# Kernel tuning notes

Measured on AMD Instinct MI355X. Metric: run time of the kernel, lower is better.

## Reference

```python
import jax, jax.numpy as jnp
import numpy as np

N = 20000      # nodes
E = 640000     # edges
D_IN = 128
D_OUT = 128
EPS_LN = 1e-6


def setup_inputs() -> dict:
    key = jax.random.key(0)
    ks = jax.random.split(key, 12)
    h = jax.random.normal(ks[0], (N, D_IN), dtype=jnp.float32)
    r = jax.random.normal(ks[1], (E, D_IN), dtype=jnp.float32)
    src = jax.random.randint(ks[2], (E,), 0, N, dtype=jnp.int32)
    dst = jax.random.randint(ks[3], (E,), 0, N, dtype=jnp.int32)
    # LayerNorm params (head, tail, rel)
    hn_a = jnp.ones((D_IN,), jnp.float32); hn_b = jnp.zeros((D_IN,), jnp.float32)
    tn_a = jnp.ones((D_IN,), jnp.float32); tn_b = jnp.zeros((D_IN,), jnp.float32)
    rn_a = jnp.ones((D_IN,), jnp.float32); rn_b = jnp.zeros((D_IN,), jnp.float32)
    sc = 1.0 / np.sqrt(D_IN)
    head_w = jax.random.normal(ks[4], (D_IN,), jnp.float32) * sc
    tail_w = jax.random.normal(ks[5], (D_IN,), jnp.float32) * sc
    rel_w = jax.random.normal(ks[6], (D_IN,), jnp.float32) * sc
    fc_w = jax.random.normal(ks[7], (D_IN, D_OUT), jnp.float32) * sc
    fc_b = jnp.zeros((D_OUT,), jnp.float32)
    return {"h": h, "r": r, "src": src, "dst": dst,
            "hn_a": hn_a, "hn_b": hn_b, "tn_a": tn_a, "tn_b": tn_b,
            "rn_a": rn_a, "rn_b": rn_b,
            "head_w": head_w, "tail_w": tail_w, "rel_w": rel_w,
            "fc_w": fc_w, "fc_b": fc_b}


def _layer_norm(x, a, b):
    # faithful to torch: std with Bessel correction (unbiased), eps added to std
    mean = x.mean(axis=-1, keepdims=True)
    var = jnp.sum((x - mean) ** 2, axis=-1, keepdims=True) / (x.shape[-1] - 1)
    std = jnp.sqrt(var)
    return a * (x - mean) / (std + EPS_LN) + b


def reference(h, r, src, dst, hn_a, hn_b, tn_a, tn_b, rn_a, rn_b,
              head_w, tail_w, rel_w, fc_w, fc_b):
    # per-node / per-edge scalar attention logits
    eh = jnp.tanh(_layer_norm(h, hn_a, hn_b) @ head_w)   # [N]
    et = jnp.tanh(_layer_norm(h, tn_a, tn_b) @ tail_w)   # [N]
    er = jnp.tanh(_layer_norm(r, rn_a, rn_b) @ rel_w)    # [E]
    # edge attention: act(eh[src] + et[dst] + er), activation = relu
    e = jax.nn.relu(eh[src] + et[dst] + er)              # [E]
    # edge_softmax: softmax over incoming edges of each destination node
    emax = jax.ops.segment_max(e, dst, num_segments=N)   # [N]
    ex = jnp.exp(e - emax[dst])
    esum = jax.ops.segment_sum(ex, dst, num_segments=N)  # [N]
    a = ex / esum[dst]                                   # [E]
    # u_mul_e + sum aggregation: feat[v] = sum_{(u->v)} a_e * h[u]
    msg = h[src] * a[:, None]                            # [E, D_IN]
    feat = jax.ops.segment_sum(msg, dst, num_segments=N) # [N, D_IN]
    out = feat @ fc_w + fc_b                             # [N, D_OUT]
    # F.normalize(p=2, dim=1)
    nrm = jnp.sqrt(jnp.sum(out * out, axis=1, keepdims=True))
    return out / jnp.maximum(nrm, 1e-12)
```

## Files before the change

kernel.cpp:

```cpp
#include <hip/hip_runtime.h>
#include <stdint.h>

#define D_DIM 128
#define EPS_LN 1e-6f

__device__ __forceinline__ float tanh_fast(float x) {
    return 1.0f - 2.0f / (__expf(2.0f * x) + 1.0f);
}

__device__ __forceinline__ float wave_sum(float v) {
    #pragma unroll
    for (int m = 1; m < 64; m <<= 1) v += __shfl_xor(v, m, 64);
    return v;
}

__device__ __forceinline__ float group16_sum(float v) {
    #pragma unroll
    for (int m = 1; m < 16; m <<= 1) v += __shfl_xor(v, m, 64);
    return v;
}

__device__ __forceinline__ float dot8_ln(const float4& a, const float4& b,
                                         float mean, float inv,
                                         const float4& wa0, const float4& wa1,
                                         const float4& wb0, const float4& wb1,
                                         const float4& ww0, const float4& ww1) {
    float p = 0.0f;
    p += ((a.x - mean) * inv * wa0.x + wb0.x) * ww0.x;
    p += ((a.y - mean) * inv * wa0.y + wb0.y) * ww0.y;
    p += ((a.z - mean) * inv * wa0.z + wb0.z) * ww0.z;
    p += ((a.w - mean) * inv * wa0.w + wb0.w) * ww0.w;
    p += ((b.x - mean) * inv * wa1.x + wb1.x) * ww1.x;
    p += ((b.y - mean) * inv * wa1.y + wb1.y) * ww1.y;
    p += ((b.z - mean) * inv * wa1.z + wb1.z) * ww1.z;
    p += ((b.w - mean) * inv * wa1.w + wb1.w) * ww1.w;
    return p;
}

__global__ __launch_bounds__(256) void k_node(
    const float* __restrict__ h,
    const float* __restrict__ hn_a, const float* __restrict__ hn_b,
    const float* __restrict__ tn_a, const float* __restrict__ tn_b,
    const float* __restrict__ head_w, const float* __restrict__ tail_w,
    float* __restrict__ eh, float* __restrict__ et, int n)
{
    int gid  = blockIdx.x * 256 + threadIdx.x;
    int node = gid >> 4;
    int sub  = threadIdx.x & 15;
    if (node >= n) return;

    const float4* hp = (const float4*)(h + (size_t)node * 128);
    float4 a = hp[sub * 2], b = hp[sub * 2 + 1];

    float s  = a.x + a.y + a.z + a.w + b.x + b.y + b.z + b.w;
    float s2 = a.x*a.x + a.y*a.y + a.z*a.z + a.w*a.w
             + b.x*b.x + b.y*b.y + b.z*b.z + b.w*b.w;
    s  = group16_sum(s);
    s2 = group16_sum(s2);
    float mean = s * (1.0f / 128.0f);
    float var  = fmaxf((s2 - s * mean) * (1.0f / 127.0f), 0.0f);
    float inv  = 1.0f / (sqrtf(var) + EPS_LN);

    int i0 = sub * 2, i1 = sub * 2 + 1;
    float4 ha0 = ((const float4*)hn_a)[i0],  ha1 = ((const float4*)hn_a)[i1];
    float4 hb0 = ((const float4*)hn_b)[i0],  hb1 = ((const float4*)hn_b)[i1];
    float4 hw0 = ((const float4*)head_w)[i0],hw1 = ((const float4*)head_w)[i1];
    float4 ta0 = ((const float4*)tn_a)[i0],  ta1 = ((const float4*)tn_a)[i1];
    float4 tb0 = ((const float4*)tn_b)[i0],  tb1 = ((const float4*)tn_b)[i1];
    float4 tw0 = ((const float4*)tail_w)[i0],tw1 = ((const float4*)tail_w)[i1];

    float ph = dot8_ln(a, b, mean, inv, ha0, ha1, hb0, hb1, hw0, hw1);
    float pt = dot8_ln(a, b, mean, inv, ta0, ta1, tb0, tb1, tw0, tw1);
    ph = group16_sum(ph);
    pt = group16_sum(pt);

    if (sub == 0) {
        eh[node] = tanh_fast(ph);
        et[node] = tanh_fast(pt);
    }
}

__global__ __launch_bounds__(256) void k_edge(
    const float* __restrict__ r,
    const float* __restrict__ rn_a, const float* __restrict__ rn_b,
    const float* __restrict__ rel_w,
    const int* __restrict__ src, const int* __restrict__ dst,
    const float* __restrict__ eh, const float* __restrict__ et,
    float* __restrict__ e_x, int* __restrict__ cnt, int nE)
{
    int gid  = blockIdx.x * 256 + threadIdx.x;
    int edge = gid >> 4;
    int sub  = threadIdx.x & 15;
    if (edge >= nE) return;

    int sN = 0, dN = 0;
    float vh = 0.0f, vt = 0.0f;
    if (sub == 0) {
        sN = src[edge];
        dN = dst[edge];
        vh = eh[sN];
        vt = et[dN];
    }

    const float4* rp = (const float4*)(r + (size_t)edge * 128);
    float4 a = rp[sub * 2], b = rp[sub * 2 + 1];

    float s  = a.x + a.y + a.z + a.w + b.x + b.y + b.z + b.w;
    float s2 = a.x*a.x + a.y*a.y + a.z*a.z + a.w*a.w
             + b.x*b.x + b.y*b.y + b.z*b.z + b.w*b.w;
    s  = group16_sum(s);
    s2 = group16_sum(s2);
    float mean = s * (1.0f / 128.0f);
    float var  = fmaxf((s2 - s * mean) * (1.0f / 127.0f), 0.0f);
    float inv  = 1.0f / (sqrtf(var) + EPS_LN);

    int i0 = sub * 2, i1 = sub * 2 + 1;
    float4 ra0 = ((const float4*)rn_a)[i0],  ra1 = ((const float4*)rn_a)[i1];
    float4 rb0 = ((const float4*)rn_b)[i0],  rb1 = ((const float4*)rn_b)[i1];
    float4 rw0 = ((const float4*)rel_w)[i0], rw1 = ((const float4*)rel_w)[i1];

    float pr = dot8_ln(a, b, mean, inv, ra0, ra1, rb0, rb1, rw0, rw1);
    pr = group16_sum(pr);

    if (sub == 0) {
        float v = tanh_fast(pr) + vh + vt;
        v = fmaxf(v, 0.0f);
        e_x[edge] = __expf(v);
        atomicAdd(cnt + dN, 1);
    }
}

__global__ __launch_bounds__(1024) void k_scan(
    const int* __restrict__ cnt, int* __restrict__ off, int* __restrict__ cursor, int n)
{
    __shared__ int wsum[16];
    __shared__ int carry_s;
    int tid = threadIdx.x, lane = tid & 63, wid = tid >> 6;
    if (tid == 0) carry_s = 0;
    __syncthreads();
    int nC = (n + 1023) >> 10;
    for (int c = 0; c < nC; c++) {
        int i = (c << 10) + tid;
        int v = (i < n) ? cnt[i] : 0;
        int x = v;
        #pragma unroll
        for (int s = 1; s < 64; s <<= 1) {
            int t = __shfl_up(x, s, 64);
            if (lane >= s) x += t;
        }
        if (lane == 63) wsum[wid] = x;
        __syncthreads();
        if (wid == 0 && lane < 16) {
            int y = wsum[lane];
            #pragma unroll
            for (int s = 1; s < 16; s <<= 1) {
                int t = __shfl_up(y, s, 64);
                if (lane >= s) y += t;
            }
            wsum[lane] = y;
        }
        __syncthreads();
        int waveoff = (wid == 0) ? 0 : wsum[wid - 1];
        int excl = carry_s + waveoff + x - v;
        if (i < n) { off[i] = excl; cursor[i] = excl; }
        int tot = wsum[15];
        __syncthreads();
        if (tid == 0) carry_s += tot;
    }
    if (threadIdx.x == 0) off[n] = carry_s;
}

__global__ __launch_bounds__(256) void k_scatter(
    const int* __restrict__ src, const int* __restrict__ dst,
    const float* __restrict__ e_x, int* __restrict__ cursor,
    int* __restrict__ ssrc, float* __restrict__ sex, int nE)
{
    int e = blockIdx.x * 256 + threadIdx.x;
    if (e >= nE) return;
    int d = dst[e];
    int slot = atomicAdd(cursor + d, 1);
    ssrc[slot] = src[e];
    sex[slot]  = e_x[e];
}

__global__ __launch_bounds__(256) void k_agg(
    const float* __restrict__ h,
    const int* __restrict__ off,
    const int* __restrict__ ssrc, const float* __restrict__ sex,
    const float* __restrict__ fc_w, const float* __restrict__ fc_b,
    float* __restrict__ out, int n)
{
    __shared__ float feat[4][128];
    int wid = threadIdx.x >> 6, lane = threadIdx.x & 63;
    int v = blockIdx.x * 4 + wid;
    if (v >= n) return;

    int beg = off[v], end = off[v + 1];
    const float2* h2 = (const float2*)h;

    float acc0 = 0.0f, acc1 = 0.0f;
    float acc2 = 0.0f, acc3 = 0.0f;
    float ws0 = 0.0f, ws1 = 0.0f;

    for (int i = beg; i < end; i += 8) {
        int m = end - i;
        int   s_[8];
        float w_[8];
        float2 p_[8];
        #pragma unroll
        for (int j = 0; j < 8; j++) {
            if (j < m) { s_[j] = ssrc[i + j]; w_[j] = sex[i + j]; }
        }
        #pragma unroll
        for (int j = 0; j < 8; j++) {
            if (j < m) p_[j] = h2[(size_t)s_[j] * 64 + lane];
        }
        #pragma unroll
        for (int j = 0; j < 8; j += 2) {
            if (j < m) {
                acc0 += w_[j] * p_[j].x;
                acc1 += w_[j] * p_[j].y;
                ws0  += w_[j];
            }
            if (j + 1 < m) {
                acc2 += w_[j + 1] * p_[j + 1].x;
                acc3 += w_[j + 1] * p_[j + 1].y;
                ws1  += w_[j + 1];
            }
        }
    }
    acc0 += acc2; acc1 += acc3;
    float ws = ws0 + ws1;

    float inv = (end > beg) ? (1.0f / ws) : 0.0f;
    feat[wid][lane * 2]     = acc0 * inv;
    feat[wid][lane * 2 + 1] = acc1 * inv;

    const float2* w2 = (const float2*)fc_w;
    float2 bb = ((const float2*)fc_b)[lane];
    float o0 = bb.x, o1 = bb.y;
    #pragma unroll 8
    for (int d = 0; d < 128; d++) {
        float f = feat[wid][d];
        float2 ww = w2[d * 64 + lane];
        o0 += f * ww.x;
        o1 += f * ww.y;
    }

    float nrm2 = wave_sum(o0 * o0 + o1 * o1);
    float invn = 1.0f / fmaxf(sqrtf(nrm2), 1e-12f);
    o0 *= invn; o1 *= invn;
    float2 q; q.x = o0; q.y = o1;
    ((float2*)out)[(size_t)v * 64 + lane] = q;
}

extern "C" void kernel_launch(void* const* d_in, const int* in_sizes, int n_in,
                              void* d_out, int out_size, void* d_ws, size_t ws_size,
                              hipStream_t stream)
{
    const float* h      = (const float*)d_in[0];
    const float* r      = (const float*)d_in[1];
    const int*   src    = (const int*)d_in[2];
    const int*   dst    = (const int*)d_in[3];
    const float* hn_a   = (const float*)d_in[4];
    const float* hn_b   = (const float*)d_in[5];
    const float* tn_a   = (const float*)d_in[6];
    const float* tn_b   = (const float*)d_in[7];
    const float* rn_a   = (const float*)d_in[8];
    const float* rn_b   = (const float*)d_in[9];
    const float* head_w = (const float*)d_in[10];
    const float* tail_w = (const float*)d_in[11];
    const float* rel_w  = (const float*)d_in[12];
    const float* fc_w   = (const float*)d_in[13];
    const float* fc_b   = (const float*)d_in[14];

    int N = in_sizes[0] / D_DIM;
    int E = in_sizes[2];

    const int NA = 20480;
    float* base   = (float*)d_ws;
    float* eh     = base;
    float* et     = base + NA;
    int*   cnt    = (int*)(base + 2 * NA);
    int*   off    = (int*)(base + 3 * NA);
    int*   cursor = (int*)(base + 4 * NA);
    float* e_x    = base + 5 * NA;
    int*   ssrc   = (int*)(base + 5 * NA) + E;
    float* sex    = base + 5 * NA + 2 * E;

    hipMemsetAsync(cnt, 0, (size_t)NA * sizeof(int), stream);

    k_node<<<(N * 16 + 255) / 256, 256, 0, stream>>>(
        h, hn_a, hn_b, tn_a, tn_b, head_w, tail_w, eh, et, N);
    k_edge<<<(E * 16 + 255) / 256, 256, 0, stream>>>(
        r, rn_a, rn_b, rel_w, src, dst, eh, et, e_x, cnt, E);
    k_scan<<<1, 1024, 0, stream>>>(cnt, off, cursor, N);
    k_scatter<<<(E + 255) / 256, 256, 0, stream>>>(src, dst, e_x, cursor, ssrc, sex, E);
    k_agg<<<(N + 3) / 4, 256, 0, stream>>>(h, off, ssrc, sex, fc_w, fc_b,
                                           (float*)d_out, N);
}
```

Before: 645.1 us.

## Fuse all GNN stages into one cooperative persistent kernel with grid syncs

Merges the node-logit, edge-logit, scan, scatter and aggregation kernels plus the memset into a single cooperative launch. Grid-wide syncs separate the stages, and every stage uses grid-stride loops over an occupancy-sized grid. The edge pass now records each edge's atomic rank within its destination, so the scatter needs no second atomic. The single-block scan becomes a multi-block two-level scan, and source index and weight are packed into one int2 for the gather. This removes launch gaps and the serial scan, at the cost of five grid barriers and occupancy limited to what allows co-residency.

```diff
diff --git a/kernel.cpp b/kernel.cpp
--- a/kernel.cpp
+++ b/kernel.cpp
@@ -1,8 +1,12 @@
 #include <hip/hip_runtime.h>
+#include <hip/hip_cooperative_groups.h>
 #include <stdint.h>
+
+namespace cg = cooperative_groups;
 
 #define D_DIM 128
 #define EPS_LN 1e-6f
+#define NA 20480
 
 __device__ __forceinline__ float tanh_fast(float x) {
     return 1.0f - 2.0f / (__expf(2.0f * x) + 1.0f);
@@ -37,221 +41,220 @@
     return p;
 }
 
-__global__ __launch_bounds__(256) void k_node(
-    const float* __restrict__ h,
+__global__ __launch_bounds__(256) void k_fused(
+    const float* __restrict__ h, const float* __restrict__ r,
+    const int* __restrict__ src, const int* __restrict__ dst,
     const float* __restrict__ hn_a, const float* __restrict__ hn_b,
     const float* __restrict__ tn_a, const float* __restrict__ tn_b,
+    const float* __restrict__ rn_a, const float* __restrict__ rn_b,
     const float* __restrict__ head_w, const float* __restrict__ tail_w,
-    float* __restrict__ eh, float* __restrict__ et, int n)
+    const float* __restrict__ rel_w,
+    const float* __restrict__ fc_w, const float* __restrict__ fc_b,
+    float* __restrict__ out, float* __restrict__ ws,
+    int n, int nE)
 {
-    int gid  = blockIdx.x * 256 + threadIdx.x;
-    int node = gid >> 4;
-    int sub  = threadIdx.x & 15;
-    if (node >= n) return;
-
-    const float4* hp = (const float4*)(h + (size_t)node * 128);
-    float4 a = hp[sub * 2], b = hp[sub * 2 + 1];
-
-    float s  = a.x + a.y + a.z + a.w + b.x + b.y + b.z + b.w;
-    float s2 = a.x*a.x + a.y*a.y + a.z*a.z + a.w*a.w
-             + b.x*b.x + b.y*b.y + b.z*b.z + b.w*b.w;
-    s  = group16_sum(s);
-    s2 = group16_sum(s2);
-    float mean = s * (1.0f / 128.0f);
-    float var  = fmaxf((s2 - s * mean) * (1.0f / 127.0f), 0.0f);
-    float inv  = 1.0f / (sqrtf(var) + EPS_LN);
-
-    int i0 = sub * 2, i1 = sub * 2 + 1;
-    float4 ha0 = ((const float4*)hn_a)[i0],  ha1 = ((const float4*)hn_a)[i1];
-    float4 hb0 = ((const float4*)hn_b)[i0],  hb1 = ((const float4*)hn_b)[i1];
-    float4 hw0 = ((const float4*)head_w)[i0],hw1 = ((const float4*)head_w)[i1];
-    float4 ta0 = ((const float4*)tn_a)[i0],  ta1 = ((const float4*)tn_a)[i1];
-    float4 tb0 = ((const float4*)tn_b)[i0],  tb1 = ((const float4*)tn_b)[i1];
-    float4 tw0 = ((const float4*)tail_w)[i0],tw1 = ((const float4*)tail_w)[i1];
-
-    float ph = dot8_ln(a, b, mean, inv, ha0, ha1, hb0, hb1, hw0, hw1);
-    float pt = dot8_ln(a, b, mean, inv, ta0, ta1, tb0, tb1, tw0, tw1);
-    ph = group16_sum(ph);
-    pt = group16_sum(pt);
-
-    if (sub == 0) {
-        eh[node] = tanh_fast(ph);
-        et[node] = tanh_fast(pt);
-    }
-}
-
-__global__ __launch_bounds__(256) void k_edge(
-    const float* __restrict__ r,
-    const float* __restrict__ rn_a, const float* __restrict__ rn_b,
-    const float* __restrict__ rel_w,
-    const int* __restrict__ src, const int* __restrict__ dst,
-    const float* __restrict__ eh, const float* __restrict__ et,
-    float* __restrict__ e_x, int* __restrict__ cnt, int nE)
-{
-    int gid  = blockIdx.x * 256 + threadIdx.x;
-    int edge = gid >> 4;
-    int sub  = threadIdx.x & 15;
-    if (edge >= nE) return;
-
-    int sN = 0, dN = 0;
-    float vh = 0.0f, vt = 0.0f;
-    if (sub == 0) {
-        sN = src[edge];
-        dN = dst[edge];
-        vh = eh[sN];
-        vt = et[dN];
-    }
-
-    const float4* rp = (const float4*)(r + (size_t)edge * 128);
-    float4 a = rp[sub * 2], b = rp[sub * 2 + 1];
-
-    float s  = a.x + a.y + a.z + a.w + b.x + b.y + b.z + b.w;
-    float s2 = a.x*a.x + a.y*a.y + a.z*a.z + a.w*a.w
-             + b.x*b.x + b.y*b.y + b.z*b.z + b.w*b.w;
-    s  = group16_sum(s);
-    s2 = group16_sum(s2);
-    float mean = s * (1.0f / 128.0f);
-    float var  = fmaxf((s2 - s * mean) * (1.0f / 127.0f), 0.0f);
-    float inv  = 1.0f / (sqrtf(var) + EPS_LN);
-
-    int i0 = sub * 2, i1 = sub * 2 + 1;
-    float4 ra0 = ((const float4*)rn_a)[i0],  ra1 = ((const float4*)rn_a)[i1];
-    float4 rb0 = ((const float4*)rn_b)[i0],  rb1 = ((const float4*)rn_b)[i1];
-    float4 rw0 = ((const float4*)rel_w)[i0], rw1 = ((const float4*)rel_w)[i1];
-
-    float pr = dot8_ln(a, b, mean, inv, ra0, ra1, rb0, rb1, rw0, rw1);
-    pr = group16_sum(pr);
-
-    if (sub == 0) {
-        float v = tanh_fast(pr) + vh + vt;
-        v = fmaxf(v, 0.0f);
-        e_x[edge] = __expf(v);
-        atomicAdd(cnt + dN, 1);
-    }
-}
-
-__global__ __launch_bounds__(1024) void k_scan(
-    const int* __restrict__ cnt, int* __restrict__ off, int* __restrict__ cursor, int n)
-{
-    __shared__ int wsum[16];
-    __shared__ int carry_s;
-    int tid = threadIdx.x, lane = tid & 63, wid = tid >> 6;
-    if (tid == 0) carry_s = 0;
-    __syncthreads();
-    int nC = (n + 1023) >> 10;
-    for (int c = 0; c < nC; c++) {
-        int i = (c << 10) + tid;
+    cg::grid_group gg = cg::this_grid();
+
+    float* eh   = ws;
+    float* et   = ws + NA;
+    int*   cnt  = (int*)(ws + 2 * NA);
+    int*   offl = (int*)(ws + 3 * NA);
+    int*   bsum = (int*)(ws + 4 * NA);
+    int*   bpre = bsum + 256;
+    int2*  emeta = (int2*)(ws + 4 * NA + 512);
+    int2*  edata = emeta + nE;
+
+    const int gthreads = gridDim.x * 256;
+    const int gtid = blockIdx.x * 256 + threadIdx.x;
+    const int sub  = threadIdx.x & 15;
+
+    __shared__ float feat[4][128];
+    __shared__ int sscan[4];
+
+    for (int i = gtid; i < NA; i += gthreads) cnt[i] = 0;
+
+    for (int unit = gtid; unit < n * 16; unit += gthreads) {
+        int node = unit >> 4;
+        const float4* hp = (const float4*)(h + (size_t)node * 128);
+        float4 a = hp[sub * 2], b = hp[sub * 2 + 1];
+
+        float s  = a.x + a.y + a.z + a.w + b.x + b.y + b.z + b.w;
+        float s2 = a.x*a.x + a.y*a.y + a.z*a.z + a.w*a.w
+                 + b.x*b.x + b.y*b.y + b.z*b.z + b.w*b.w;
+        s  = group16_sum(s);
+        s2 = group16_sum(s2);
+        float mean = s * (1.0f / 128.0f);
+        float var  = fmaxf((s2 - s * mean) * (1.0f / 127.0f), 0.0f);
+        float inv  = 1.0f / (sqrtf(var) + EPS_LN);
+
+        int i0 = sub * 2, i1 = sub * 2 + 1;
+        float4 ha0 = ((const float4*)hn_a)[i0],  ha1 = ((const float4*)hn_a)[i1];
+        float4 hb0 = ((const float4*)hn_b)[i0],  hb1 = ((const float4*)hn_b)[i1];
+        float4 hw0 = ((const float4*)head_w)[i0],hw1 = ((const float4*)head_w)[i1];
+        float4 ta0 = ((const float4*)tn_a)[i0],  ta1 = ((const float4*)tn_a)[i1];
+        float4 tb0 = ((const float4*)tn_b)[i0],  tb1 = ((const float4*)tn_b)[i1];
+        float4 tw0 = ((const float4*)tail_w)[i0],tw1 = ((const float4*)tail_w)[i1];
+
+        float ph = dot8_ln(a, b, mean, inv, ha0, ha1, hb0, hb1, hw0, hw1);
+        float pt = dot8_ln(a, b, mean, inv, ta0, ta1, tb0, tb1, tw0, tw1);
+        ph = group16_sum(ph);
+        pt = group16_sum(pt);
+        if (sub == 0) {
+            eh[node] = tanh_fast(ph);
+            et[node] = tanh_fast(pt);
+        }
+    }
+    gg.sync();
+
+    for (int unit = gtid; unit < nE * 16; unit += gthreads) {
+        int edge = unit >> 4;
+        int sN = 0, dN = 0;
+        float vh = 0.0f, vt = 0.0f;
+        if (sub == 0) {
+            sN = src[edge]; dN = dst[edge];
+            vh = eh[sN];    vt = et[dN];
+        }
+        const float4* rp = (const float4*)(r + (size_t)edge * 128);
+        float4 a = rp[sub * 2], b = rp[sub * 2 + 1];
+
+        float s  = a.x + a.y + a.z + a.w + b.x + b.y + b.z + b.w;
+        float s2 = a.x*a.x + a.y*a.y + a.z*a.z + a.w*a.w
+                 + b.x*b.x + b.y*b.y + b.z*b.z + b.w*b.w;
+        s  = group16_sum(s);
+        s2 = group16_sum(s2);
+        float mean = s * (1.0f / 128.0f);
+        float var  = fmaxf((s2 - s * mean) * (1.0f / 127.0f), 0.0f);
+        float inv  = 1.0f / (sqrtf(var) + EPS_LN);
+
+        int i0 = sub * 2, i1 = sub * 2 + 1;
+        float4 ra0 = ((const float4*)rn_a)[i0],  ra1 = ((const float4*)rn_a)[i1];
+        float4 rb0 = ((const float4*)rn_b)[i0],  rb1 = ((const float4*)rn_b)[i1];
+        float4 rw0 = ((const float4*)rel_w)[i0], rw1 = ((const float4*)rel_w)[i1];
+
+        float pr = dot8_ln(a, b, mean, inv, ra0, ra1, rb0, rb1, rw0, rw1);
+        pr = group16_sum(pr);
+
+        if (sub == 0) {
+            float v = tanh_fast(pr) + vh + vt;
+            v = fmaxf(v, 0.0f);
+            int rank = atomicAdd(cnt + dN, 1);
+            emeta[edge] = make_int2(rank, __float_as_int(__expf(v)));
+        }
+    }
+    gg.sync();
+
+    const int B1 = (n + 256) >> 8;
+    for (int b = blockIdx.x; b < B1; b += gridDim.x) {
+        int i = (b << 8) + threadIdx.x;
         int v = (i < n) ? cnt[i] : 0;
+        int lane = threadIdx.x & 63, w4 = threadIdx.x >> 6;
         int x = v;
         #pragma unroll
         for (int s = 1; s < 64; s <<= 1) {
             int t = __shfl_up(x, s, 64);
             if (lane >= s) x += t;
         }
-        if (lane == 63) wsum[wid] = x;
-        __syncthreads();
-        if (wid == 0 && lane < 16) {
-            int y = wsum[lane];
-            #pragma unroll
-            for (int s = 1; s < 16; s <<= 1) {
-                int t = __shfl_up(y, s, 64);
-                if (lane >= s) y += t;
+        if (lane == 63) sscan[w4] = x;
+        __syncthreads();
+        if (threadIdx.x == 0) {
+            int a0 = sscan[0], a1 = sscan[1], a2 = sscan[2], a3 = sscan[3];
+            sscan[0] = 0; sscan[1] = a0; sscan[2] = a0 + a1; sscan[3] = a0 + a1 + a2;
+            bsum[b] = a0 + a1 + a2 + a3;
+        }
+        __syncthreads();
+        offl[i] = sscan[w4] + x - v;
+        __syncthreads();
+    }
+    gg.sync();
+
+    if (blockIdx.x == 0) {
+        int t = threadIdx.x;
+        int v = (t < B1) ? bsum[t] : 0;
+        int lane = t & 63, w4 = t >> 6;
+        int x = v;
+        #pragma unroll
+        for (int s = 1; s < 64; s <<= 1) {
+            int tt = __shfl_up(x, s, 64);
+            if (lane >= s) x += tt;
+        }
+        if (lane == 63) sscan[w4] = x;
+        __syncthreads();
+        if (t == 0) {
+            int a0 = sscan[0], a1 = sscan[1], a2 = sscan[2], a3 = sscan[3];
+            sscan[0] = 0; sscan[1] = a0; sscan[2] = a0 + a1; sscan[3] = a0 + a1 + a2;
+        }
+        __syncthreads();
+        bpre[t] = sscan[w4] + x - v;
+    }
+    gg.sync();
+
+    for (int e = gtid; e < nE; e += gthreads) {
+        int d = dst[e];
+        int2 m = emeta[e];
+        int slot = offl[d] + bpre[d >> 8] + m.x;
+        edata[slot] = make_int2(src[e], m.y);
+    }
+    gg.sync();
+
+    {
+        int gw = gtid >> 6, lane = gtid & 63, wid = threadIdx.x >> 6;
+        int nwaves = gthreads >> 6;
+        const float2* h2 = (const float2*)h;
+        const float2* w2 = (const float2*)fc_w;
+        float2 bb = ((const float2*)fc_b)[lane];
+
+        for (int v = gw; v < n; v += nwaves) {
+            int beg = offl[v]     + bpre[v >> 8];
+            int end = offl[v + 1] + bpre[(v + 1) >> 8];
+
+            float acc0 = 0.0f, acc1 = 0.0f;
+            float acc2 = 0.0f, acc3 = 0.0f;
+            float ws0 = 0.0f, ws1 = 0.0f;
+
+            for (int i = beg; i < end; i += 8) {
+                int m = end - i;
+                int2   q_[8];
+                float2 p_[8];
+                #pragma unroll
+                for (int j = 0; j < 8; j++)
+                    if (j < m) q_[j] = edata[i + j];
+                #pragma unroll
+                for (int j = 0; j < 8; j++)
+                    if (j < m) p_[j] = h2[(size_t)q_[j].x * 64 + lane];
+                #pragma unroll
+                for (int j = 0; j < 8; j += 2) {
+                    if (j < m) {
+                        float w = __int_as_float(q_[j].y);
+                        acc0 += w * p_[j].x; acc1 += w * p_[j].y; ws0 += w;
+                    }
+                    if (j + 1 < m) {
+                        float w = __int_as_float(q_[j + 1].y);
+                        acc2 += w * p_[j + 1].x; acc3 += w * p_[j + 1].y; ws1 += w;
+                    }
+                }
             }
-            wsum[lane] = y;
-        }
-        __syncthreads();
-        int waveoff = (wid == 0) ? 0 : wsum[wid - 1];
-        int excl = carry_s + waveoff + x - v;
-        if (i < n) { off[i] = excl; cursor[i] = excl; }
-        int tot = wsum[15];
-        __syncthreads();
-        if (tid == 0) carry_s += tot;
-    }
-    if (threadIdx.x == 0) off[n] = carry_s;
-}
-
-__global__ __launch_bounds__(256) void k_scatter(
-    const int* __restrict__ src, const int* __restrict__ dst,
-    const float* __restrict__ e_x, int* __restrict__ cursor,
-    int* __restrict__ ssrc, float* __restrict__ sex, int nE)
-{
-    int e = blockIdx.x * 256 + threadIdx.x;
-    if (e >= nE) return;
-    int d = dst[e];
-    int slot = atomicAdd(cursor + d, 1);
-    ssrc[slot] = src[e];
-    sex[slot]  = e_x[e];
-}
-
-__global__ __launch_bounds__(256) void k_agg(
-    const float* __restrict__ h,
-    const int* __restrict__ off,
-    const int* __restrict__ ssrc, const float* __restrict__ sex,
-    const float* __restrict__ fc_w, const float* __restrict__ fc_b,
-    float* __restrict__ out, int n)
-{
-    __shared__ float feat[4][128];
-    int wid = threadIdx.x >> 6, lane = threadIdx.x & 63;
-    int v = blockIdx.x * 4 + wid;
-    if (v >= n) return;
-
-    int beg = off[v], end = off[v + 1];
-    const float2* h2 = (const float2*)h;
-
-    float acc0 = 0.0f, acc1 = 0.0f;
-    float acc2 = 0.0f, acc3 = 0.0f;
-    float ws0 = 0.0f, ws1 = 0.0f;
-
-    for (int i = beg; i < end; i += 8) {
-        int m = end - i;
-        int   s_[8];
-        float w_[8];
-        float2 p_[8];
-        #pragma unroll
-        for (int j = 0; j < 8; j++) {
-            if (j < m) { s_[j] = ssrc[i + j]; w_[j] = sex[i + j]; }
-        }
-        #pragma unroll
-        for (int j = 0; j < 8; j++) {
-            if (j < m) p_[j] = h2[(size_t)s_[j] * 64 + lane];
-        }
-        #pragma unroll
-        for (int j = 0; j < 8; j += 2) {
-            if (j < m) {
-                acc0 += w_[j] * p_[j].x;
-                acc1 += w_[j] * p_[j].y;
-                ws0  += w_[j];
+            acc0 += acc2; acc1 += acc3;
+            float wsum = ws0 + ws1;
+
+            float inv = (end > beg) ? (1.0f / wsum) : 0.0f;
+            feat[wid][lane * 2]     = acc0 * inv;
+            feat[wid][lane * 2 + 1] = acc1 * inv;
+
+            float o0 = bb.x, o1 = bb.y;
+            #pragma unroll 8
+            for (int d = 0; d < 128; d++) {
+                float f = feat[wid][d];
+                float2 ww = w2[d * 64 + lane];
+                o0 += f * ww.x;
+                o1 += f * ww.y;
             }
-            if (j + 1 < m) {
-                acc2 += w_[j + 1] * p_[j + 1].x;
-                acc3 += w_[j + 1] * p_[j + 1].y;
-                ws1  += w_[j + 1];
-            }
-        }
-    }
-    acc0 += acc2; acc1 += acc3;
-    float ws = ws0 + ws1;
-
-    float inv = (end > beg) ? (1.0f / ws) : 0.0f;
-    feat[wid][lane * 2]     = acc0 * inv;
-    feat[wid][lane * 2 + 1] = acc1 * inv;
-
-    const float2* w2 = (const float2*)fc_w;
-    float2 bb = ((const float2*)fc_b)[lane];
-    float o0 = bb.x, o1 = bb.y;
-    #pragma unroll 8
-    for (int d = 0; d < 128; d++) {
-        float f = feat[wid][d];
-        float2 ww = w2[d * 64 + lane];
-        o0 += f * ww.x;
-        o1 += f * ww.y;
-    }
-
-    float nrm2 = wave_sum(o0 * o0 + o1 * o1);
-    float invn = 1.0f / fmaxf(sqrtf(nrm2), 1e-12f);
-    o0 *= invn; o1 *= invn;
-    float2 q; q.x = o0; q.y = o1;
-    ((float2*)out)[(size_t)v * 64 + lane] = q;
+
+            float nrm2 = wave_sum(o0 * o0 + o1 * o1);
+            float invn = 1.0f / fmaxf(sqrtf(nrm2), 1e-12f);
+            float2 q; q.x = o0 * invn; q.y = o1 * invn;
+            ((float2*)out)[(size_t)v * 64 + lane] = q;
+        }
+    }
 }
 
 extern "C" void kernel_launch(void* const* d_in, const int* in_sizes, int n_in,
@@ -277,25 +280,29 @@
     int N = in_sizes[0] / D_DIM;
     int E = in_sizes[2];
 
-    const int NA = 20480;
-    float* base   = (float*)d_ws;
-    float* eh     = base;
-    float* et     = base + NA;
-    int*   cnt    = (int*)(base + 2 * NA);
-    int*   off    = (int*)(base + 3 * NA);
-    int*   cursor = (int*)(base + 4 * NA);
-    float* e_x    = base + 5 * NA;
-    int*   ssrc   = (int*)(base + 5 * NA) + E;
-    float* sex    = base + 5 * NA + 2 * E;
-
-    hipMemsetAsync(cnt, 0, (size_t)NA * sizeof(int), stream);
-
-    k_node<<<(N * 16 + 255) / 256, 256, 0, stream>>>(
-        h, hn_a, hn_b, tn_a, tn_b, head_w, tail_w, eh, et, N);
-    k_edge<<<(E * 16 + 255) / 256, 256, 0, stream>>>(
-        r, rn_a, rn_b, rel_w, src, dst, eh, et, e_x, cnt, E);
-    k_scan<<<1, 1024, 0, stream>>>(cnt, off, cursor, N);
-    k_scatter<<<(E + 255) / 256, 256, 0, stream>>>(src, dst, e_x, cursor, ssrc, sex, E);
-    k_agg<<<(N + 3) / 4, 256, 0, stream>>>(h, off, ssrc, sex, fc_w, fc_b,
-                                           (float*)d_out, N);
-}
+    float* outp = (float*)d_out;
+    float* wsp  = (float*)d_ws;
+
+    static int gblocks = 0;
+    if (gblocks == 0) {
+        int occ = 0;
+        hipOccupancyMaxActiveBlocksPerMultiprocessor(&occ, k_fused, 256, 0);
+        if (occ < 1) occ = 1;
+        hipDeviceProp_t prop;
+        hipGetDeviceProperties(&prop, 0);
+        gblocks = occ * prop.multiProcessorCount;
+        if (gblocks > 2048) gblocks = 2048;
+        if (gblocks < 128)  gblocks = 128;
+    }
+
+    void* args[] = {
+        (void*)&h, (void*)&r, (void*)&src, (void*)&dst,
+        (void*)&hn_a, (void*)&hn_b, (void*)&tn_a, (void*)&tn_b,
+        (void*)&rn_a, (void*)&rn_b,
+        (void*)&head_w, (void*)&tail_w, (void*)&rel_w,
+        (void*)&fc_w, (void*)&fc_b,
+        (void*)&outp, (void*)&wsp, (void*)&N, (void*)&E };
+
+    hipLaunchCooperativeKernel((const void*)k_fused, dim3(gblocks), dim3(256),
+                               args, 0, stream);
+}
```

New measurement: 1.062 ms. +64.6%, slower.
